# Performance work log

Measured on AMD Instinct MI355X. Metric: run time of the kernel, lower is better.

Reference implementation:

```python
import jax, jax.numpy as jnp
import numpy as np

B, L, K = 4, 4096, 48
BIG = 1e9  # masked-out distance sentinel


def setup_inputs() -> dict:
    key = jax.random.key(0)
    k1, k2 = jax.random.split(key)
    # Backbone coords (B, L, 4, 3): N, CA, C, O. Scaled to Angstrom-ish magnitudes.
    X = jax.random.normal(k1, (B, L, 4, 3), dtype=jnp.float32) * 10.0
    mask = (jax.random.uniform(k2, (B, L)) > 0.1).astype(jnp.float32)
    return {"X": X, "mask": mask, "k_neighbors": K}


def reference(X, mask, k_neighbors):
    """GPU-friendly equivalent of precompute_knn_cpu:
    brute-force masked pairwise euclidean distances + top-k, with
    self-fill for invalid residues and the degenerate n_valid<=k batch case.
    Returns (D_neighbors (B,L,k) float, E_idx (B,L,k) int32).
    """
    Xca = X[:, :, 1, :]                       # (B, L, 3) CA atoms
    m = mask > 0                              # (B, L) bool valid
    # ||a-b||^2 = ||a||^2 + ||b||^2 - 2 a.b  (avoids (B,L,L,3) intermediate)
    x2 = jnp.sum(Xca * Xca, axis=-1)          # (B, L)
    D2 = x2[:, :, None] + x2[:, None, :] - 2.0 * jnp.einsum('bld,bmd->blm', Xca, Xca)
    D = jnp.sqrt(jnp.maximum(D2, 0.0))        # (B, L, L)
    # mask invalid key columns so they are never selected
    Dm = jnp.where(m[:, None, :], D, BIG)
    _, idx = jax.lax.top_k(-Dm, k_neighbors)  # k smallest distances, (B, L, k)
    self_idx = jnp.broadcast_to(jnp.arange(L, dtype=idx.dtype)[None, :, None],
                                (B, L, k_neighbors))
    n_valid = jnp.sum(m, axis=1)              # (B,)
    # degenerate batch: n_valid <= k -> every row filled with its own index
    degen = (n_valid <= k_neighbors)[:, None, None]
    # invalid rows -> self index; valid rows -> knn indices (already in original index space)
    E_idx = jnp.where(degen | (~m[:, :, None]), self_idx, idx)
    D_neighbors = jnp.take_along_axis(D, E_idx, axis=2)  # (B, L, k)
    return D_neighbors, E_idx
```

## Files before the change

### kernel.cpp

```cpp
#include <hip/hip_runtime.h>

typedef unsigned long long u64;

#define L_DIM 4096
#define B_DIM 4
#define KNN 48
#define CAP 512
#define INVALID_X2 1.0e30f
#define VALID_TH 1.0e29f
#define SLACK 8u
#define NT 256
#define NW 4
#define CPT 16
#define ROWS 2

__global__ __launch_bounds__(256) void prep_kernel(const float* __restrict__ X,
                                                   const float* __restrict__ mask,
                                                   float4* __restrict__ c4) {
#pragma clang fp contract(off)
    int i = blockIdx.x * 256 + threadIdx.x;
    const float4* X4 = (const float4*)X;
    float4 a = X4[3 * i];
    float4 bb = X4[3 * i + 1];
    float x = a.w, y = bb.x, z = bb.y;
    float x2 = __builtin_fmaf(z, z, __builtin_fmaf(y, y, x * x));
    float m = mask[i];
    c4[i] = make_float4(x, y, z, (m > 0.0f) ? x2 : INVALID_X2);
}

__device__ __forceinline__ unsigned wave_sort64(unsigned sv, int lane) {
#pragma unroll
    for (int k = 2; k <= 64; k <<= 1) {
#pragma unroll
        for (int j = k >> 1; j > 0; j >>= 1) {
            unsigned o = __shfl_xor(sv, j);
            unsigned mn = min(sv, o), mx = max(sv, o);
            bool asc = ((lane & k) == 0);
            bool low = ((lane & j) == 0);
            sv = (asc == low) ? mn : mx;
        }
    }
    return sv;
}

__global__ __launch_bounds__(NT) void knn_kernel(const float4* __restrict__ c4,
                                                 float* __restrict__ dn,
                                                 float* __restrict__ ei) {
    __shared__ u64 smin[ROWS][NT];
    __shared__ u64 surv[ROWS][CAP];
    __shared__ int nvw[NW];
    __shared__ int cnt[ROWS];
    __shared__ unsigned Tsh[ROWS];

    const int row0 = blockIdx.x * ROWS;
    const int b = row0 >> 12;
    const int i0 = row0 & (L_DIM - 1);
    const int t = threadIdx.x;
    const int w = t >> 6, lane = t & 63;

    const float4* cb = c4 + (size_t)b * L_DIM;
    const float4 q0 = cb[i0];
    const float4 q1 = cb[i0 + 1];
    const bool v0 = (q0.w < VALID_TH), v1 = (q1.w < VALID_TH);

    unsigned d20[CPT], d21[CPT];
    unsigned rmin0 = 0xFFFFFFFFu, rmin1 = 0xFFFFFFFFu;
    int nvt = 0;
    {
#pragma clang fp contract(off)
#pragma unroll
        for (int c = 0; c < CPT; ++c) {
            int j = c * NT + t;
            float4 pj = cb[j];
            nvt += (pj.w < VALID_TH) ? 1 : 0;
            float dota = __builtin_fmaf(pj.z, q0.z,
                         __builtin_fmaf(pj.y, q0.y, pj.x * q0.x));
            float dotb = __builtin_fmaf(pj.z, q1.z,
                         __builtin_fmaf(pj.y, q1.y, pj.x * q1.x));
            float d2a = fmaxf(__builtin_fmaf(-2.0f, dota, q0.w + pj.w), 0.0f);
            float d2b = fmaxf(__builtin_fmaf(-2.0f, dotb, q1.w + pj.w), 0.0f);
            d20[c] = __float_as_uint(d2a);
            d21[c] = __float_as_uint(d2b);
            rmin0 = min(rmin0, d20[c]);
            rmin1 = min(rmin1, d21[c]);
        }
    }

#pragma unroll
    for (int s = 1; s < 64; s <<= 1) nvt += __shfl_xor(nvt, s);
    if (lane == 0) nvw[w] = nvt;
    if (t < ROWS) cnt[t] = 0;
    __syncthreads();
    if (nvw[0] + nvw[1] + nvw[2] + nvw[3] <= KNN) {
        if (w < ROWS && lane < KNN) {
            dn[(size_t)(row0 + w) * KNN + lane] = 0.0f;
            ei[(size_t)(row0 + w) * KNN + lane] = (float)(i0 + w);
        }
        return;
    }

    {
        unsigned sv0 = wave_sort64(rmin0, lane);
        unsigned sv1 = wave_sort64(rmin1, lane);
        smin[0][t] = ((u64)sv0 << 32) | (unsigned)t;
        smin[1][t] = ((u64)sv1 << 32) | (unsigned)t;
    }
    __syncthreads();

    for (int tau = t; tau < ROWS * NW * KNN; tau += NT) {
        int r = tau / (NW * KNN);
        int rest = tau - r * (NW * KNN);
        int ww = rest / KNN, p = rest - ww * KNN;
        u64 key = smin[r][ww * 64 + p];
        int grank = p;
#pragma unroll
        for (int w2 = 0; w2 < NW; ++w2) {
            if (w2 == ww) continue;
            const u64* arr = &smin[r][w2 * 64];
            int lo = 0;
#pragma unroll
            for (int s = 32; s >= 1; s >>= 1)
                if (arr[lo + s - 1] < key) lo += s;
            lo += (arr[lo] < key) ? 1 : 0;
            grank += lo;
        }
        if (grank == KNN - 1) Tsh[r] = (unsigned)(key >> 32);
    }
    __syncthreads();
    const unsigned Tp0 = v0 ? (Tsh[0] + SLACK) : 0u;
    const unsigned Tp1 = v1 ? (Tsh[1] + SLACK) : 0u;

#pragma unroll
    for (int c = 0; c < CPT; ++c) {
        unsigned j = (unsigned)(c * NT + t);
        if (d20[c] <= Tp0) {
            int pos = atomicAdd(&cnt[0], 1);
            if (pos < CAP) {
                float d = sqrtf(__uint_as_float(d20[c]));
                surv[0][pos] = ((u64)__float_as_uint(d) << 32) | j;
            }
        }
        if (d21[c] <= Tp1) {
            int pos = atomicAdd(&cnt[1], 1);
            if (pos < CAP) {
                float d = sqrtf(__uint_as_float(d21[c]));
                surv[1][pos] = ((u64)__float_as_uint(d) << 32) | j;
            }
        }
    }
    __syncthreads();

#pragma unroll
    for (int r = 0; r < ROWS; ++r) {
        const bool vr = r ? v1 : v0;
        float* dnrow = dn + (size_t)(row0 + r) * KNN;
        float* eirow = ei + (size_t)(row0 + r) * KNN;
        if (!vr) {
            if (t < KNN) { dnrow[t] = 0.0f; eirow[t] = (float)(i0 + r); }
        } else {
            int S = cnt[r]; if (S > CAP) S = CAP;
            for (int c = t; c < S; c += NT) {
                u64 key = surv[r][c];
                int rank = 0;
                for (int s = 0; s < S; ++s) rank += (surv[r][s] < key);
                if (rank < KNN) {
                    dnrow[rank] = __uint_as_float((unsigned)(key >> 32));
                    eirow[rank] = (float)(key & 0xFFFFFFFFULL);
                }
            }
        }
    }
}

extern "C" void kernel_launch(void* const* d_in, const int* in_sizes, int n_in,
                              void* d_out, int out_size, void* d_ws, size_t ws_size,
                              hipStream_t stream) {
    const float* X = (const float*)d_in[0];
    const float* mask = (const float*)d_in[1];

    float* out = (float*)d_out;
    float* dn = out;
    float* ei = out + (size_t)B_DIM * L_DIM * KNN;

    float4* c4 = (float4*)d_ws;

    prep_kernel<<<(B_DIM * L_DIM) / 256, 256, 0, stream>>>(X, mask, c4);
    knn_kernel<<<(B_DIM * L_DIM) / ROWS, NT, 0, stream>>>(c4, dn, ei);
}
```

Before: 81.51 us.

## Precompute per-batch valid counts and derive threshold from grouped minima with one sort

The prep kernel now counts valid residues per batch with a ballot and an atomic, so the knn kernel can exit early on degenerate batches without a per-block reduction. The selection threshold changes: each group of 4 threads reduces to one minimum, and a single 64-lane bitonic sort per row takes the 48th smallest group minimum. This replaces the per-wave sorts and the cross-wave binary-search ranking, and drops one barrier. In exchange the threshold is looser, so more survivors reach the quadratic rank pass and the CAP buffer fills more. It also adds a memset launch and global atomics.

Measured after the change: 72.09 us. 1.13x faster.

```diff
diff --git a/kernel.cpp b/kernel.cpp
--- a/kernel.cpp
+++ b/kernel.cpp
@@ -16,7 +16,8 @@
 
 __global__ __launch_bounds__(256) void prep_kernel(const float* __restrict__ X,
                                                    const float* __restrict__ mask,
-                                                   float4* __restrict__ c4) {
+                                                   float4* __restrict__ c4,
+                                                   int* __restrict__ nvalid) {
 #pragma clang fp contract(off)
     int i = blockIdx.x * 256 + threadIdx.x;
     const float4* X4 = (const float4*)X;
@@ -26,6 +27,9 @@
     float x2 = __builtin_fmaf(z, z, __builtin_fmaf(y, y, x * x));
     float m = mask[i];
     c4[i] = make_float4(x, y, z, (m > 0.0f) ? x2 : INVALID_X2);
+    unsigned long long bal = __ballot(m > 0.0f);
+    if ((threadIdx.x & 63) == 0)
+        atomicAdd(&nvalid[i >> 12], (int)__popcll(bal));
 }
 
 __device__ __forceinline__ unsigned wave_sort64(unsigned sv, int lane) {
@@ -44,11 +48,11 @@
 }
 
 __global__ __launch_bounds__(NT) void knn_kernel(const float4* __restrict__ c4,
+                                                 const int* __restrict__ nvalid,
                                                  float* __restrict__ dn,
                                                  float* __restrict__ ei) {
-    __shared__ u64 smin[ROWS][NT];
+    __shared__ unsigned gmin[ROWS][64];
     __shared__ u64 surv[ROWS][CAP];
-    __shared__ int nvw[NW];
     __shared__ int cnt[ROWS];
     __shared__ unsigned Tsh[ROWS];
 
@@ -58,6 +62,14 @@
     const int t = threadIdx.x;
     const int w = t >> 6, lane = t & 63;
 
+    if (nvalid[b] <= KNN) {
+        if (w < ROWS && lane < KNN) {
+            dn[(size_t)(row0 + w) * KNN + lane] = 0.0f;
+            ei[(size_t)(row0 + w) * KNN + lane] = (float)(i0 + w);
+        }
+        return;
+    }
+
     const float4* cb = c4 + (size_t)b * L_DIM;
     const float4 q0 = cb[i0];
     const float4 q1 = cb[i0 + 1];
@@ -65,14 +77,12 @@
 
     unsigned d20[CPT], d21[CPT];
     unsigned rmin0 = 0xFFFFFFFFu, rmin1 = 0xFFFFFFFFu;
-    int nvt = 0;
     {
 #pragma clang fp contract(off)
 #pragma unroll
         for (int c = 0; c < CPT; ++c) {
             int j = c * NT + t;
             float4 pj = cb[j];
-            nvt += (pj.w < VALID_TH) ? 1 : 0;
             float dota = __builtin_fmaf(pj.z, q0.z,
                          __builtin_fmaf(pj.y, q0.y, pj.x * q0.x));
             float dotb = __builtin_fmaf(pj.z, q1.z,
@@ -86,45 +96,21 @@
         }
     }
 
-#pragma unroll
-    for (int s = 1; s < 64; s <<= 1) nvt += __shfl_xor(nvt, s);
-    if (lane == 0) nvw[w] = nvt;
+    {
+        unsigned g0 = min(rmin0, __shfl_xor(rmin0, 1));
+        g0 = min(g0, __shfl_xor(g0, 2));
+        unsigned g1 = min(rmin1, __shfl_xor(rmin1, 1));
+        g1 = min(g1, __shfl_xor(g1, 2));
+        if ((lane & 3) == 0) {
+            gmin[0][(w << 4) | (lane >> 2)] = g0;
+            gmin[1][(w << 4) | (lane >> 2)] = g1;
+        }
+    }
     if (t < ROWS) cnt[t] = 0;
     __syncthreads();
-    if (nvw[0] + nvw[1] + nvw[2] + nvw[3] <= KNN) {
-        if (w < ROWS && lane < KNN) {
-            dn[(size_t)(row0 + w) * KNN + lane] = 0.0f;
-            ei[(size_t)(row0 + w) * KNN + lane] = (float)(i0 + w);
-        }
-        return;
-    }
-
-    {
-        unsigned sv0 = wave_sort64(rmin0, lane);
-        unsigned sv1 = wave_sort64(rmin1, lane);
-        smin[0][t] = ((u64)sv0 << 32) | (unsigned)t;
-        smin[1][t] = ((u64)sv1 << 32) | (unsigned)t;
-    }
-    __syncthreads();
-
-    for (int tau = t; tau < ROWS * NW * KNN; tau += NT) {
-        int r = tau / (NW * KNN);
-        int rest = tau - r * (NW * KNN);
-        int ww = rest / KNN, p = rest - ww * KNN;
-        u64 key = smin[r][ww * 64 + p];
-        int grank = p;
-#pragma unroll
-        for (int w2 = 0; w2 < NW; ++w2) {
-            if (w2 == ww) continue;
-            const u64* arr = &smin[r][w2 * 64];
-            int lo = 0;
-#pragma unroll
-            for (int s = 32; s >= 1; s >>= 1)
-                if (arr[lo + s - 1] < key) lo += s;
-            lo += (arr[lo] < key) ? 1 : 0;
-            grank += lo;
-        }
-        if (grank == KNN - 1) Tsh[r] = (unsigned)(key >> 32);
+    if (w < ROWS) {
+        unsigned sv = wave_sort64(gmin[w][lane], lane);
+        if (lane == KNN - 1) Tsh[w] = sv;
     }
     __syncthreads();
     const unsigned Tp0 = v0 ? (Tsh[0] + SLACK) : 0u;
@@ -182,8 +168,11 @@
     float* dn = out;
     float* ei = out + (size_t)B_DIM * L_DIM * KNN;
 
-    float4* c4 = (float4*)d_ws;
+    char* ws = (char*)d_ws;
+    float4* c4 = (float4*)ws;
+    int* nv = (int*)(ws + (size_t)B_DIM * L_DIM * 16);
 
-    prep_kernel<<<(B_DIM * L_DIM) / 256, 256, 0, stream>>>(X, mask, c4);
-    knn_kernel<<<(B_DIM * L_DIM) / ROWS, NT, 0, stream>>>(c4, dn, ei);
+    hipMemsetAsync(nv, 0, B_DIM * sizeof(int), stream);
+    prep_kernel<<<(B_DIM * L_DIM) / 256, 256, 0, stream>>>(X, mask, c4, nv);
+    knn_kernel<<<(B_DIM * L_DIM) / ROWS, NT, 0, stream>>>(c4, nv, dn, ei);
 }
```
